# Optimization experiments

Hardware: AMD Instinct MI355X
Metric: run time of the kernel (lower is better)

Reference implementation:

```python
import jax, jax.numpy as jnp
import numpy as np

ALPHA = 0.5            # conf['alpha'] hybrid mixing
MAX_TOP_ANT = 50       # conf['max_top_antecedents']
MAX_SPAN_WIDTH = 30


def bucket_distance(d):
    # util.bucket_distance: identity 0..4, then log2 buckets, clipped to [0, 9]
    logspace = jnp.floor(jnp.log2(jnp.maximum(d, 1).astype(jnp.float32))).astype(d.dtype) + 3
    return jnp.clip(jnp.where(d <= 4, d, logspace), 0, 9)


def setup_inputs() -> dict:
    key = jax.random.key(0)
    ks = jax.random.split(key, 16)
    W, D, K, F, H = 4096, 768, 768, 20, 1000
    SPAN = 3 * D                      # span_emb_size = 3 * bert_emb_size
    PAIR = 3 * SPAN + F               # pair_emb_size (use_features only)
    std = 0.02

    mention_doc = jax.random.normal(ks[0], (W, D), jnp.float32)
    mention_doc_one = jax.random.normal(ks[1], (W, D), jnp.float32)
    top_span_starts = jnp.sort(jax.random.randint(ks[2], (K,), 0, W - MAX_SPAN_WIDTH))
    widths = jax.random.randint(ks[3], (K,), 0, MAX_SPAN_WIDTH)
    top_span_ends = jnp.minimum(top_span_starts + widths, W - 1)
    top_span_mention_scores = jax.random.normal(ks[4], (K,), jnp.float32)

    return {
        "mention_doc": mention_doc,
        "mention_doc_one": mention_doc_one,
        "top_span_starts": top_span_starts,
        "top_span_ends": top_span_ends,
        "top_span_mention_scores": top_span_mention_scores,
        # mention_token_attn: Linear(D -> 1)
        "attn_w": jax.random.normal(ks[5], (D,), jnp.float32) * std,
        "attn_b": jnp.zeros((), jnp.float32),
        # coarse_bilinear: Linear(SPAN -> SPAN)
        "coarse_w": jax.random.normal(ks[6], (SPAN, SPAN), jnp.float32) * std,
        "coarse_b": jnp.zeros((SPAN,), jnp.float32),
        # emb_antecedent_distance_prior [10, F] + antecedent_distance_score_ffnn Linear(F -> 1)
        "dist_prior_emb": jax.random.normal(ks[7], (10, F), jnp.float32) * std,
        "dist_w": jax.random.normal(ks[8], (F,), jnp.float32) * std,
        "dist_b": jnp.zeros((), jnp.float32),
        # emb_top_antecedent_distance [10, F]
        "top_dist_emb": jax.random.normal(ks[9], (10, F), jnp.float32) * std,
        # coref_score_ffnn: Linear(PAIR -> H), ReLU, Linear(H -> 1)
        "coref_w1": jax.random.normal(ks[10], (PAIR, H), jnp.float32) * std,
        "coref_b1": jnp.zeros((H,), jnp.float32),
        "coref_w2": jax.random.normal(ks[11], (H,), jnp.float32) * std,
        "coref_b2": jnp.zeros((), jnp.float32),
    }


def reference(mention_doc, mention_doc_one, top_span_starts, top_span_ends,
              top_span_mention_scores, attn_w, attn_b, coarse_w, coarse_b,
              dist_prior_emb, dist_w, dist_b, top_dist_emb,
              coref_w1, coref_b1, coref_w2, coref_b2):
    W = mention_doc.shape[0]
    K = top_span_starts.shape[0]
    C = min(K, MAX_TOP_ANT)
    NEG_INF = jnp.float32(-1e30) * 0 - jnp.inf  # true -inf, matches torch.log(0.)

    # --- span embeddings: start / end / head-attention over hybrid doc ---
    start_emb = mention_doc[top_span_starts]                      # [K, D]
    end_emb = mention_doc[top_span_ends]                          # [K, D]
    hybrid = mention_doc * (1.0 - ALPHA) + mention_doc_one * ALPHA
    token_attn = hybrid @ attn_w + attn_b                         # [W]
    tok = jnp.arange(W)
    span_tok_mask = (tok[None, :] >= top_span_starts[:, None]) & \
                    (tok[None, :] <= top_span_ends[:, None])      # [K, W]
    attn_raw = jnp.where(span_tok_mask, token_attn[None, :], NEG_INF)
    attn_probs = jax.nn.softmax(attn_raw, axis=1)                 # [K, W]
    head_emb = attn_probs @ hybrid                                # [K, D]
    span_emb = jnp.concatenate([start_emb, end_emb, head_emb], axis=1)  # [K, 3D]

    # --- coarse (fast) pairwise scores ---
    rng = jnp.arange(K)
    ant_offsets = rng[:, None] - rng[None, :]                     # [K, K]
    ant_mask = ant_offsets >= 1
    pair_sum = top_span_mention_scores[:, None] + top_span_mention_scores[None, :]
    src = span_emb @ coarse_w + coarse_b                          # coarse_bilinear
    fast = pair_sum + src @ span_emb.T
    fast = jnp.where(ant_mask, fast, NEG_INF)                     # + log(mask)
    dist_score = dist_prior_emb @ dist_w + dist_b                 # [10]
    fast = fast + dist_score[bucket_distance(ant_offsets)]        # distance prior

    # --- top-k antecedent pruning ---
    top_fast, top_idx = jax.lax.top_k(fast, C)                    # [K, C]
    top_ant_offsets = jnp.take_along_axis(ant_offsets, top_idx, axis=1)

    # --- fine-grained pairwise FFNN scoring ---
    dist_emb = top_dist_emb[bucket_distance(top_ant_offsets)]     # [K, C, F]
    ant_emb = span_emb[top_idx]                                   # [K, C, 3D]
    tgt_emb = jnp.broadcast_to(span_emb[:, None, :], ant_emb.shape)
    sim_emb = span_emb[:, None, :] * ant_emb
    pair_emb = jnp.concatenate([tgt_emb, ant_emb, sim_emb, dist_emb], axis=-1)  # [K, C, PAIR]
    h = jax.nn.relu(jnp.einsum('kcp,ph->kch', pair_emb, coref_w1) + coref_b1)
    slow = jnp.einsum('kch,h->kc', h, coref_w2) + coref_b2        # [K, C]
    top_scores = slow + top_fast

    # dummy antecedent (epsilon) column of zeros
    return jnp.concatenate([jnp.zeros((K, 1), top_scores.dtype), top_scores], axis=1)
```

## Files before the change

kernel.cpp:

```cpp
#include <hip/hip_runtime.h>
#include <math.h>

#define WTOK 4096
#define DD   768
#define KK   768
#define SPAN 2304
#define HH   1000
#define CC   50
#define NPAD 1024
#define NBIG 4352
#define PROWS (KK * CC)
#define PCHUNK (PROWS * 4)

typedef __attribute__((ext_vector_type(8))) short bf16x8;
typedef __attribute__((ext_vector_type(4))) float f32x4;
typedef unsigned short ushort;
typedef unsigned int uint;

__device__ __forceinline__ int bucketd(int d) {
  int l = (d >= 1) ? (31 - __clz(d)) : 0;
  int v = (d <= 4) ? d : (l + 3);
  return min(max(v, 0), 9);
}
__device__ __forceinline__ ushort f2bf(float f) {
  uint u = __float_as_uint(f);
  return (ushort)((u + 0x7fffu + ((u >> 16) & 1u)) >> 16);
}
__device__ __forceinline__ uint pkmul_t(uint a, uint b) {
  float lo = __uint_as_float(a << 16) * __uint_as_float(b << 16);
  float hi = __uint_as_float(a & 0xffff0000u) * __uint_as_float(b & 0xffff0000u);
  return (__float_as_uint(lo) >> 16) | (__float_as_uint(hi) & 0xffff0000u);
}
__device__ __forceinline__ uint4 pkmul4(uint4 a, uint4 b) {
  uint4 r;
  r.x = pkmul_t(a.x, b.x); r.y = pkmul_t(a.y, b.y);
  r.z = pkmul_t(a.z, b.z); r.w = pkmul_t(a.w, b.w);
  return r;
}
__device__ __forceinline__ void dma16(const ushort* g, ushort* l) {
  __builtin_amdgcn_global_load_lds(
      (const __attribute__((address_space(1))) void*)g,
      (__attribute__((address_space(3))) void*)l, 16, 0, 0);
}

#define PB_COARSE 5184
#define PB_W 2304
#define PB_SETUP_BASE (PB_COARSE + 3 * PB_W)
#define PB_SLOW_BASE  (PB_SETUP_BASE + 40)
#define PB_TOTAL      (PB_SLOW_BASE + 150)

__global__ __launch_bounds__(256) void prep_k(
    const float* __restrict__ coarse_w, const float* __restrict__ W1,
    const float* __restrict__ dist_prior, const float* __restrict__ dist_w,
    const float* __restrict__ dist_b, const float* __restrict__ top_dist,
    ushort* __restrict__ BigT, ushort* __restrict__ W1simT,
    float* __restrict__ dist_score, float* __restrict__ Pdist,
    float* __restrict__ slow)
{
  int bid = blockIdx.x;
  int tid = threadIdx.x;
  if (bid >= PB_SLOW_BASE) {
    int t = (bid - PB_SLOW_BASE) * 256 + tid;
    if (t < KK * CC) slow[t] = 0.f;
    return;
  }
  if (bid >= PB_SETUP_BASE) {
    int t = (bid - PB_SETUP_BASE) * 256 + tid;
    if (t < 10) {
      float s = dist_b[0];
      for (int f = 0; f < 20; ++f) s += dist_prior[t * 20 + f] * dist_w[f];
      dist_score[t] = s;
    }
    if (t < 10 * HH) {
      int b = t / HH, h = t % HH;
      float s = 0.f;
      for (int f = 0; f < 20; ++f)
        s += top_dist[b * 20 + f] * W1[(long)(6912 + f) * HH + h];
      Pdist[t] = s;
    }
    return;
  }
  const float* in; int ldin, Cin, nbase, NBrows; ushort* out; int idx;
  int xt;
  if (bid < PB_COARSE) {
    idx = bid; in = coarse_w; ldin = SPAN; Cin = SPAN; nbase = 0;
    NBrows = NBIG; out = BigT; xt = SPAN / 32;
  } else {
    idx = bid - PB_COARSE;
    int region = idx / PB_W;
    idx = idx % PB_W;
    if (region == 0) { in = W1; nbase = 2304; NBrows = NBIG; out = BigT; }
    else if (region == 1) { in = W1 + (size_t)SPAN * HH; nbase = 3328; NBrows = NBIG; out = BigT; }
    else { in = W1 + (size_t)2 * SPAN * HH; nbase = 0; NBrows = NPAD; out = W1simT; }
    ldin = HH; Cin = HH; xt = NPAD / 32;
  }
  {
    int bx = idx % xt, by = idx / xt;
    __shared__ float tile[32][33];
    int n0 = bx * 32, p0 = by * 32;
    int tx = tid & 31, ty = tid >> 5;
    for (int i = ty; i < 32; i += 8) {
      int p = p0 + i, n = n0 + tx;
      tile[i][tx] = (n < Cin) ? in[(long)p * ldin + n] : 0.f;
    }
    __syncthreads();
    size_t slab = (size_t)(p0 >> 5) * NBrows * 32;
    for (int i = ty; i < 32; i += 8) {
      int n = n0 + i;
      out[slab + (size_t)(nbase + n) * 32 + tx] = f2bf(tile[tx][i]);
    }
  }
}

__global__ __launch_bounds__(256) void hybrid_attn_k(
    const float* __restrict__ doc, const float* __restrict__ doc1,
    const float* __restrict__ attn_w, const float* __restrict__ attn_b,
    float* __restrict__ hybrid, float* __restrict__ tok_attn)
{
  int w = blockIdx.x;
  int tid = threadIdx.x;
  float part = 0.f;
  for (int d = tid; d < DD; d += 256) {
    float h = 0.5f * doc[(long)w * DD + d] + 0.5f * doc1[(long)w * DD + d];
    hybrid[(long)w * DD + d] = h;
    part += h * attn_w[d];
  }
  for (int off = 32; off > 0; off >>= 1) part += __shfl_down(part, off, 64);
  __shared__ float ws4[4];
  if ((tid & 63) == 0) ws4[tid >> 6] = part;
  __syncthreads();
  if (tid == 0) tok_attn[w] = ws4[0] + ws4[1] + ws4[2] + ws4[3] + attn_b[0];
}

__global__ __launch_bounds__(256) void span_emb_k(
    const float* __restrict__ doc, const float* __restrict__ hybrid,
    const float* __restrict__ tok_attn, const int* __restrict__ starts,
    const int* __restrict__ ends, ushort* __restrict__ se_bf)
{
  int k = blockIdx.x;
  int s = starts[k], e = ends[k];
  int len = e - s + 1;
  int tid = threadIdx.x;
  __shared__ float p_s[32];
  if (tid < 32) {
    float v = (tid < len) ? tok_attn[s + tid] : -INFINITY;
    float m = v;
    for (int msk = 16; msk >= 1; msk >>= 1) m = fmaxf(m, __shfl_xor(m, msk, 32));
    float pe = (tid < len) ? expf(v - m) : 0.f;
    float Z = pe;
    for (int msk = 16; msk >= 1; msk >>= 1) Z += __shfl_xor(Z, msk, 32);
    p_s[tid] = pe / Z;
  }
  __syncthreads();
  for (int d = tid; d < DD; d += 256) {
    float h = 0.f;
    for (int t = 0; t < len; ++t) h += p_s[t] * hybrid[(long)(s + t) * DD + d];
    se_bf[(long)k * SPAN + d]          = f2bf(doc[(long)s * DD + d]);
    se_bf[(long)k * SPAN + DD + d]     = f2bf(doc[(long)e * DD + d]);
    se_bf[(long)k * SPAN + 2 * DD + d] = f2bf(h);
  }
}

__global__ __launch_bounds__(256) void gemm_combined_k(
    const ushort* __restrict__ A, const ushort* __restrict__ B,
    const float* __restrict__ coarse_b, const float* __restrict__ b1,
    ushort* __restrict__ src_bf, float* __restrict__ Ptgt,
    float* __restrict__ Pant)
{
  __shared__ __align__(16) ushort As[64 * 40];
  __shared__ __align__(16) ushort Bs[128 * 32];
  int tid = threadIdx.x;
  int m0 = blockIdx.x * 64, n0 = blockIdx.y * 128;
  int lane = tid & 63, wid = tid >> 6;
  int quad = lane >> 4, lr = lane & 15;
  int wm = (wid & 1) << 5, wn = (wid >> 1) << 6;
  int arow = tid >> 2, aq = tid & 3;
  int gofs[2];
#pragma unroll
  for (int t = 0; t < 2; ++t) {
    int S = t * 256 + tid;
    int r = S >> 2, p = S & 3;
    int q = p ^ ((r >> 1) & 3);
    gofs[t] = (n0 + r) * 32 + q * 8;
  }
  f32x4 acc[2][4] = {};
  for (int k0 = 0; k0 < SPAN; k0 += 32) {
    uint4 a0 = *(const uint4*)(A + (size_t)(m0 + arow) * SPAN + k0 + aq * 8);
    __syncthreads();
    const ushort* sb = B + (size_t)(k0 >> 5) * (NBIG * 32);
    dma16(sb + gofs[0], &Bs[(size_t)(0 * 256 + tid) * 8]);
    dma16(sb + gofs[1], &Bs[(size_t)(1 * 256 + tid) * 8]);
    *(uint4*)&As[arow * 40 + aq * 8] = a0;
    __syncthreads();
    bf16x8 af[2], bfr[4];
#pragma unroll
    for (int mi = 0; mi < 2; ++mi)
      af[mi] = *(const bf16x8*)&As[(wm + mi * 16 + lr) * 40 + quad * 8];
#pragma unroll
    for (int ni = 0; ni < 4; ++ni) {
      int r = wn + ni * 16 + lr;
      int p = quad ^ ((r >> 1) & 3);
      bfr[ni] = *(const bf16x8*)&Bs[r * 32 + p * 8];
    }
#pragma unroll
    for (int mi = 0; mi < 2; ++mi)
#pragma unroll
      for (int ni = 0; ni < 4; ++ni)
        acc[mi][ni] = __builtin_amdgcn_mfma_f32_16x16x32_bf16(
            af[mi], bfr[ni], acc[mi][ni], 0, 0, 0);
  }
#pragma unroll
  for (int mi = 0; mi < 2; ++mi)
#pragma unroll
    for (int ni = 0; ni < 4; ++ni) {
      f32x4 c = acc[mi][ni];
#pragma unroll
      for (int reg = 0; reg < 4; ++reg) {
        int gm = m0 + wm + mi * 16 + quad * 4 + reg;
        int g = n0 + wn + ni * 16 + lr;
        float v = c[reg];
        if (g < 2304) {
          src_bf[(size_t)gm * SPAN + g] = f2bf(v + coarse_b[g]);
        } else if (g < 3328) {
          int n = g - 2304;
          if (n < HH) Ptgt[(size_t)gm * HH + n] = v + b1[n];
        } else {
          int n = g - 3328;
          if (n < HH) Pant[(size_t)gm * HH + n] = v;
        }
      }
    }
}

__global__ __launch_bounds__(256) void gemm_fast_k(
    const ushort* __restrict__ A, const ushort* __restrict__ B,
    const float* __restrict__ ms, const float* __restrict__ dist_score,
    float* __restrict__ fast)
{
  __shared__ __align__(16) ushort As[64 * 40];
  __shared__ __align__(16) ushort Bs[64 * 40];
  int tid = threadIdx.x;
  int m0 = blockIdx.x * 64, n0 = blockIdx.y * 64;
  int lane = tid & 63, wid = tid >> 6;
  int quad = lane >> 4, lr = lane & 15;
  int wm = (wid & 1) << 5, wn = (wid >> 1) << 5;
  int row = tid >> 2, aq = tid & 3;
  const ushort* ga = A + (size_t)(m0 + row) * SPAN + aq * 8;
  const ushort* gb = B + (size_t)(n0 + row) * SPAN + aq * 8;
  f32x4 acc[2][2] = {};
  for (int k0 = 0; k0 < SPAN; k0 += 32) {
    uint4 a0 = *(const uint4*)(ga + k0);
    uint4 b0 = *(const uint4*)(gb + k0);
    __syncthreads();
    *(uint4*)&As[row * 40 + aq * 8] = a0;
    *(uint4*)&Bs[row * 40 + aq * 8] = b0;
    __syncthreads();
    bf16x8 af[2], bfr[2];
#pragma unroll
    for (int mi = 0; mi < 2; ++mi)
      af[mi] = *(const bf16x8*)&As[(wm + mi * 16 + lr) * 40 + quad * 8];
#pragma unroll
    for (int ni = 0; ni < 2; ++ni)
      bfr[ni] = *(const bf16x8*)&Bs[(wn + ni * 16 + lr) * 40 + quad * 8];
#pragma unroll
    for (int mi = 0; mi < 2; ++mi)
#pragma unroll
      for (int ni = 0; ni < 2; ++ni)
        acc[mi][ni] = __builtin_amdgcn_mfma_f32_16x16x32_bf16(
            af[mi], bfr[ni], acc[mi][ni], 0, 0, 0);
  }
#pragma unroll
  for (int mi = 0; mi < 2; ++mi)
#pragma unroll
    for (int ni = 0; ni < 2; ++ni) {
      f32x4 c = acc[mi][ni];
#pragma unroll
      for (int reg = 0; reg < 4; ++reg) {
        int gm = m0 + wm + mi * 16 + quad * 4 + reg;
        int gn = n0 + wn + ni * 16 + lr;
        float v;
        if (gn < gm) {
          v = c[reg] + ms[gm] + ms[gn] + dist_score[bucketd(gm - gn)];
        } else {
          v = -INFINITY;
        }
        fast[(size_t)gm * KK + gn] = v;
      }
    }
}

__global__ __launch_bounds__(256) void topk_k(
    const float* __restrict__ fast, float* __restrict__ top_fast,
    int* __restrict__ row_j, int* __restrict__ row_bucket)
{
  __shared__ float vals[KK];
  __shared__ float wbv[4];
  __shared__ int wbi[4];
  int k = blockIdx.x;
  int tid = threadIdx.x;
  for (int j = tid; j < KK; j += 256) vals[j] = fast[(long)k * KK + j];
  __syncthreads();
  const float NANF = __uint_as_float(0x7fc00000u);
  for (int it = 0; it < CC; ++it) {
    float bv = -INFINITY;
    int bi = 1 << 30;
    for (int j = tid; j < KK; j += 256) {
      float v = vals[j];
      if (v > bv || (v == bv && j < bi)) { bv = v; bi = j; }
    }
    for (int off = 32; off > 0; off >>= 1) {
      float ov = __shfl_down(bv, off, 64);
      int oi = __shfl_down(bi, off, 64);
      if (ov > bv || (ov == bv && oi < bi)) { bv = ov; bi = oi; }
    }
    if ((tid & 63) == 0) { wbv[tid >> 6] = bv; wbi[tid >> 6] = bi; }
    __syncthreads();
    if (tid == 0) {
      for (int w = 1; w < 4; ++w) {
        float ov = wbv[w]; int oi = wbi[w];
        if (ov > bv || (ov == bv && oi < bi)) { bv = ov; bi = oi; }
      }
      int r = k * CC + it;
      top_fast[r] = bv;
      row_j[r] = bi;
      row_bucket[r] = bucketd(k - bi);
      vals[bi] = NANF;
    }
    __syncthreads();
  }
}

__global__ __launch_bounds__(256) void prod_k(
    const ushort* __restrict__ se_bf, const int* __restrict__ row_j,
    ushort* __restrict__ AsimT)
{
  int u = blockIdx.x * 256 + threadIdx.x;
  int c = u / PCHUNK;
  int rem = u - c * PCHUNK;
  int r = rem >> 2;
  int q = rem & 3;
  int kidx = r / CC;
  int j = row_j[r];
  int koff = c * 32 + q * 8;
  uint4 a = *(const uint4*)(se_bf + (size_t)kidx * SPAN + koff);
  uint4 b = *(const uint4*)(se_bf + (size_t)j * SPAN + koff);
  *(uint4*)(AsimT + (size_t)c * ((size_t)PROWS * 32) + (size_t)r * 32 + q * 8) =
      pkmul4(a, b);
}

__global__ __launch_bounds__(256, 4) void pair_mfma_k(
    const ushort* __restrict__ AsimT, const ushort* __restrict__ W1simT,
    const int* __restrict__ row_j, const int* __restrict__ row_bucket,
    const float* __restrict__ Ptgt, const float* __restrict__ Pant,
    const float* __restrict__ Pdist, const float* __restrict__ w2,
    float* __restrict__ slow)
{
  __shared__ __align__(16) ushort As[2][128 * 32];
  __shared__ __align__(16) ushort Bs[2][128 * 32];
  __shared__ int ks_s[128];
  __shared__ int js_s[128];
  __shared__ int bk_s[128];
  int tid = threadIdx.x;
  int b = blockIdx.x;
  int t = (b & 7) * 300 + (b >> 3);
  int m0 = (t >> 3) * 128, n0 = (t & 7) * 128;
  if (tid < 128) {
    int r = m0 + tid;
    ks_s[tid] = r / CC;
    js_s[tid] = row_j[r];
    bk_s[tid] = row_bucket[r];
  }
  int lane = tid & 63, wid = tid >> 6;
  int quad = lane >> 4, lr = lane & 15;
  int wm = (wid & 1) << 6, wn = (wid >> 1) << 6;
  int aofs[2], bofs[2];
#pragma unroll
  for (int tt = 0; tt < 2; ++tt) {
    int S = tt * 256 + tid;
    int r = S >> 2, p = S & 3;
    int q = p ^ ((r >> 1) & 3);
    aofs[tt] = (m0 + r) * 32 + q * 8;
    bofs[tt] = (n0 + r) * 32 + q * 8;
  }
#pragma unroll
  for (int tt = 0; tt < 2; ++tt) {
    dma16(AsimT + aofs[tt],  &As[0][(size_t)(tt * 256 + tid) * 8]);
    dma16(W1simT + bofs[tt], &Bs[0][(size_t)(tt * 256 + tid) * 8]);
  }
  __syncthreads();

  f32x4 acc[4][4] = {};
  for (int k0 = 0; k0 < SPAN; k0 += 32) {
    int buf = (k0 >> 5) & 1, nb = buf ^ 1;
    bool more = (k0 + 32) < SPAN;
    if (more) {
      size_t slab = (size_t)((k0 >> 5) + 1);
#pragma unroll
      for (int tt = 0; tt < 2; ++tt) {
        dma16(AsimT + slab * ((size_t)PROWS * 32) + aofs[tt],
              &As[nb][(size_t)(tt * 256 + tid) * 8]);
        dma16(W1simT + slab * (NPAD * 32) + bofs[tt],
              &Bs[nb][(size_t)(tt * 256 + tid) * 8]);
      }
    }
    bf16x8 af[4], bfr[4];
#pragma unroll
    for (int mi = 0; mi < 4; ++mi) {
      int r = wm + mi * 16 + lr;
      int p = quad ^ ((r >> 1) & 3);
      af[mi] = *(const bf16x8*)&As[buf][r * 32 + p * 8];
    }
#pragma unroll
    for (int ni = 0; ni < 4; ++ni) {
      int r = wn + ni * 16 + lr;
      int p = quad ^ ((r >> 1) & 3);
      bfr[ni] = *(const bf16x8*)&Bs[buf][r * 32 + p * 8];
    }
#pragma unroll
    for (int ni = 0; ni < 4; ++ni)
#pragma unroll
      for (int mi = 0; mi < 4; ++mi)
        acc[mi][ni] = __builtin_amdgcn_mfma_f32_16x16x32_bf16(
            af[mi], bfr[ni], acc[mi][ni], 0, 0, 0);
    __syncthreads();
  }
  int nn[4]; float w2r[4]; bool nv[4];
#pragma unroll
  for (int ni = 0; ni < 4; ++ni) {
    nn[ni] = n0 + wn + ni * 16 + lr;
    nv[ni] = nn[ni] < HH;
    w2r[ni] = nv[ni] ? w2[nn[ni]] : 0.f;
  }
#pragma unroll
  for (int mi = 0; mi < 4; ++mi) {
#pragma unroll
    for (int reg = 0; reg < 4; ++reg) {
      int rl = wm + mi * 16 + quad * 4 + reg;
      int kk = ks_s[rl], jj = js_s[rl], bb = bk_s[rl];
      float s = 0.f;
#pragma unroll
      for (int ni = 0; ni < 4; ++ni) {
        if (nv[ni]) {
          float h = acc[mi][ni][reg] + Ptgt[(size_t)kk * HH + nn[ni]] +
                    Pant[(size_t)jj * HH + nn[ni]] +
                    Pdist[(size_t)bb * HH + nn[ni]];
          s += fmaxf(h, 0.f) * w2r[ni];
        }
      }
      s += __shfl_xor(s, 1); s += __shfl_xor(s, 2);
      s += __shfl_xor(s, 4); s += __shfl_xor(s, 8);
      if (lr == 0) atomicAdd(&slow[m0 + rl], s);
    }
  }
}

__global__ void finalize_k(const float* __restrict__ slow,
                           const float* __restrict__ top_fast,
                           const float* __restrict__ b2, float* __restrict__ out)
{
  int t = blockIdx.x * 256 + threadIdx.x;
  if (t >= KK * (CC + 1)) return;
  int k = t / (CC + 1), col = t % (CC + 1);
  if (col == 0) {
    out[t] = 0.f;
  } else {
    int r = k * CC + col - 1;
    float v = slow[r] + b2[0] + top_fast[r];
    if (!isfinite(v)) v = -1.0e30f;
    out[t] = v;
  }
}

extern "C" void kernel_launch(void* const* d_in, const int* in_sizes, int n_in,
                              void* d_out, int out_size, void* d_ws, size_t ws_size,
                              hipStream_t stream)
{
  const float* doc        = (const float*)d_in[0];
  const float* doc1       = (const float*)d_in[1];
  const int*   starts     = (const int*)d_in[2];
  const int*   ends       = (const int*)d_in[3];
  const float* ms         = (const float*)d_in[4];
  const float* attn_w     = (const float*)d_in[5];
  const float* attn_b     = (const float*)d_in[6];
  const float* coarse_w   = (const float*)d_in[7];
  const float* coarse_b   = (const float*)d_in[8];
  const float* dist_prior = (const float*)d_in[9];
  const float* dist_w     = (const float*)d_in[10];
  const float* dist_b     = (const float*)d_in[11];
  const float* top_dist   = (const float*)d_in[12];
  const float* W1         = (const float*)d_in[13];
  const float* b1         = (const float*)d_in[14];
  const float* w2         = (const float*)d_in[15];
  const float* b2         = (const float*)d_in[16];
  float* out = (float*)d_out;

  char* ws = (char*)d_ws;
  size_t off = 0;
  auto alloc = [&](size_t bytes) { void* p = ws + off; off = (off + bytes + 1023) & ~(size_t)1023; return p; };
  ushort* se_bf      = (ushort*)alloc((size_t)KK * SPAN * 2 + 4096);
  float*  Ptgt       = (float*)alloc((size_t)KK * HH * 4);
  float*  Pant       = (float*)alloc((size_t)KK * HH * 4);
  float*  Pdist      = (float*)alloc((size_t)10 * HH * 4);
  float*  dist_score = (float*)alloc(64);
  float*  top_fast   = (float*)alloc((size_t)KK * CC * 4);
  int*    row_j      = (int*)alloc((size_t)KK * CC * 4);
  int*    row_bucket = (int*)alloc((size_t)KK * CC * 4);
  float*  slow       = (float*)alloc((size_t)KK * CC * 4);
  ushort* W1simT     = (ushort*)alloc((size_t)NPAD * SPAN * 2 + 4096);
  size_t ovl = off;
  float*  hybrid     = (float*)alloc((size_t)WTOK * DD * 4);
  float*  tok_attn   = (float*)alloc((size_t)WTOK * 4);
  ushort* src_bf     = (ushort*)alloc((size_t)KK * SPAN * 2 + 4096);
  float*  fast       = (float*)alloc((size_t)KK * KK * 4);
  ushort* BigT       = (ushort*)alloc((size_t)NBIG * SPAN * 2 + 4096);
  ushort* AsimT      = (ushort*)(ws + ovl);
  (void)ws_size; (void)in_sizes; (void)n_in; (void)out_size;

  prep_k<<<PB_TOTAL, 256, 0, stream>>>(coarse_w, W1, dist_prior, dist_w,
                                       dist_b, top_dist, BigT, W1simT,
                                       dist_score, Pdist, slow);
  hybrid_attn_k<<<WTOK, 256, 0, stream>>>(doc, doc1, attn_w, attn_b, hybrid, tok_attn);
  span_emb_k<<<KK, 256, 0, stream>>>(doc, hybrid, tok_attn, starts, ends, se_bf);
  {
    dim3 g(KK / 64, NBIG / 128);
    gemm_combined_k<<<g, 256, 0, stream>>>(se_bf, BigT, coarse_b, b1,
                                           src_bf, Ptgt, Pant);
  }
  {
    dim3 g(KK / 64, KK / 64);
    gemm_fast_k<<<g, 256, 0, stream>>>(src_bf, se_bf, ms, dist_score, fast);
  }
  topk_k<<<KK, 256, 0, stream>>>(fast, top_fast, row_j, row_bucket);
  prod_k<<<(72 * PCHUNK) / 256, 256, 0, stream>>>(se_bf, row_j, AsimT);
  pair_mfma_k<<<(PROWS / 128) * (NPAD / 128), 256, 0, stream>>>(
      AsimT, W1simT, row_j, row_bucket, Ptgt, Pant, Pdist, w2, slow);
  finalize_k<<<(KK * (CC + 1) + 255) / 256, 256, 0, stream>>>(slow, top_fast, b2, out);
}
```

Before: 580.4 us.

## Enlarge pair GEMM tiles to 256x256x64 with phased MFMA/load scheduling

Rewrites the pairwise MFMA kernel to use 256x256 block tiles with BK=64 and 512 threads. It interleaves LDS reads, MFMA groups and global-to-LDS DMA stages using sched barriers and priority hints. The A and W1sim layouts change to 64-wide K slabs with an XOR swizzle to match, which updates both prod_k and the prep transpose. The intent is more data reuse per tile and better overlap of loads with compute. The costs are higher register and LDS pressure, and the epilogue now reads row metadata from global memory instead of shared.

```diff
diff --git a/kernel.cpp b/kernel.cpp
--- a/kernel.cpp
+++ b/kernel.cpp
@@ -10,7 +10,6 @@
 #define NPAD 1024
 #define NBIG 4352
 #define PROWS (KK * CC)
-#define PCHUNK (PROWS * 4)
 
 typedef __attribute__((ext_vector_type(8))) short bf16x8;
 typedef __attribute__((ext_vector_type(4))) float f32x4;
@@ -81,7 +80,7 @@
     return;
   }
   const float* in; int ldin, Cin, nbase, NBrows; ushort* out; int idx;
-  int xt;
+  int xt; bool bk64 = false;
   if (bid < PB_COARSE) {
     idx = bid; in = coarse_w; ldin = SPAN; Cin = SPAN; nbase = 0;
     NBrows = NBIG; out = BigT; xt = SPAN / 32;
@@ -91,7 +90,7 @@
     idx = idx % PB_W;
     if (region == 0) { in = W1; nbase = 2304; NBrows = NBIG; out = BigT; }
     else if (region == 1) { in = W1 + (size_t)SPAN * HH; nbase = 3328; NBrows = NBIG; out = BigT; }
-    else { in = W1 + (size_t)2 * SPAN * HH; nbase = 0; NBrows = NPAD; out = W1simT; }
+    else { in = W1 + (size_t)2 * SPAN * HH; nbase = 0; NBrows = NPAD; out = W1simT; bk64 = true; }
     ldin = HH; Cin = HH; xt = NPAD / 32;
   }
   {
@@ -104,10 +103,22 @@
       tile[i][tx] = (n < Cin) ? in[(long)p * ldin + n] : 0.f;
     }
     __syncthreads();
-    size_t slab = (size_t)(p0 >> 5) * NBrows * 32;
-    for (int i = ty; i < 32; i += 8) {
-      int n = n0 + i;
-      out[slab + (size_t)(nbase + n) * 32 + tx] = f2bf(tile[tx][i]);
+    if (!bk64) {
+      size_t slab = (size_t)(p0 >> 5) * NBrows * 32;
+      for (int i = ty; i < 32; i += 8) {
+        int n = n0 + i;
+        out[slab + (size_t)(nbase + n) * 32 + tx] = f2bf(tile[tx][i]);
+      }
+    } else {
+      int p = p0 + tx;
+      int c = p >> 6, kin = p & 63;
+      int ls = kin >> 3, e = kin & 7;
+      size_t base = (size_t)c * NPAD * 64;
+      for (int i = ty; i < 32; i += 8) {
+        int n = n0 + i;
+        int ps = ls ^ (n & 7);
+        out[base + (size_t)n * 64 + ps * 8 + e] = f2bf(tile[tx][i]);
+      }
     }
   }
 }
@@ -335,95 +346,133 @@
     ushort* __restrict__ AsimT)
 {
   int u = blockIdx.x * 256 + threadIdx.x;
-  int c = u / PCHUNK;
-  int rem = u - c * PCHUNK;
-  int r = rem >> 2;
-  int q = rem & 3;
+  int ls = u & 7;
+  int v = u >> 3;
+  int c = v / PROWS;
+  int r = v - c * PROWS;
   int kidx = r / CC;
   int j = row_j[r];
-  int koff = c * 32 + q * 8;
+  int koff = c * 64 + ls * 8;
   uint4 a = *(const uint4*)(se_bf + (size_t)kidx * SPAN + koff);
   uint4 b = *(const uint4*)(se_bf + (size_t)j * SPAN + koff);
-  *(uint4*)(AsimT + (size_t)c * ((size_t)PROWS * 32) + (size_t)r * 32 + q * 8) =
-      pkmul4(a, b);
-}
-
-__global__ __launch_bounds__(256, 4) void pair_mfma_k(
+  int ps = ls ^ (r & 7);
+  *(uint4*)(AsimT + ((size_t)c * PROWS + r) * 64 + ps * 8) = pkmul4(a, b);
+}
+
+#define BM 256
+#define BN 256
+#define BK 64
+#define KST 36
+
+#define PH_MID \
+  __builtin_amdgcn_sched_barrier(0); \
+  __builtin_amdgcn_s_barrier(); \
+  asm volatile("s_waitcnt lgkmcnt(0)" ::: "memory"); \
+  __builtin_amdgcn_sched_barrier(0); \
+  __builtin_amdgcn_s_setprio(1)
+
+#define PH_END \
+  __builtin_amdgcn_s_setprio(0); \
+  __builtin_amdgcn_sched_barrier(0); \
+  __builtin_amdgcn_s_barrier(); \
+  __builtin_amdgcn_sched_barrier(0)
+
+__global__ __launch_bounds__(512, 2) void pair_mfma_k(
     const ushort* __restrict__ AsimT, const ushort* __restrict__ W1simT,
     const int* __restrict__ row_j, const int* __restrict__ row_bucket,
     const float* __restrict__ Ptgt, const float* __restrict__ Pant,
     const float* __restrict__ Pdist, const float* __restrict__ w2,
     float* __restrict__ slow)
 {
-  __shared__ __align__(16) ushort As[2][128 * 32];
-  __shared__ __align__(16) ushort Bs[2][128 * 32];
-  __shared__ int ks_s[128];
-  __shared__ int js_s[128];
-  __shared__ int bk_s[128];
+  __shared__ __align__(16) ushort As[2][BM * BK];
+  __shared__ __align__(16) ushort Bs[2][BN * BK];
   int tid = threadIdx.x;
   int b = blockIdx.x;
-  int t = (b & 7) * 300 + (b >> 3);
-  int m0 = (t >> 3) * 128, n0 = (t & 7) * 128;
-  if (tid < 128) {
-    int r = m0 + tid;
-    ks_s[tid] = r / CC;
-    js_s[tid] = row_j[r];
-    bk_s[tid] = row_bucket[r];
-  }
+  int t = (b & 7) * 75 + (b >> 3);
+  int m0 = (t >> 2) * BM;
+  int n0 = (t & 3) * BN;
   int lane = tid & 63, wid = tid >> 6;
   int quad = lane >> 4, lr = lane & 15;
-  int wm = (wid & 1) << 6, wn = (wid >> 1) << 6;
-  int aofs[2], bofs[2];
-#pragma unroll
-  for (int tt = 0; tt < 2; ++tt) {
-    int S = tt * 256 + tid;
-    int r = S >> 2, p = S & 3;
-    int q = p ^ ((r >> 1) & 3);
-    aofs[tt] = (m0 + r) * 32 + q * 8;
-    bofs[tt] = (n0 + r) * 32 + q * 8;
-  }
-#pragma unroll
-  for (int tt = 0; tt < 2; ++tt) {
-    dma16(AsimT + aofs[tt],  &As[0][(size_t)(tt * 256 + tid) * 8]);
-    dma16(W1simT + bofs[tt], &Bs[0][(size_t)(tt * 256 + tid) * 8]);
-  }
-  __syncthreads();
-
-  f32x4 acc[4][4] = {};
-  for (int k0 = 0; k0 < SPAN; k0 += 32) {
-    int buf = (k0 >> 5) & 1, nb = buf ^ 1;
-    bool more = (k0 + 32) < SPAN;
-    if (more) {
-      size_t slab = (size_t)((k0 >> 5) + 1);
-#pragma unroll
-      for (int tt = 0; tt < 2; ++tt) {
-        dma16(AsimT + slab * ((size_t)PROWS * 32) + aofs[tt],
-              &As[nb][(size_t)(tt * 256 + tid) * 8]);
-        dma16(W1simT + slab * (NPAD * 32) + bofs[tt],
-              &Bs[nb][(size_t)(tt * 256 + tid) * 8]);
-      }
-    }
-    bf16x8 af[4], bfr[4];
-#pragma unroll
-    for (int mi = 0; mi < 4; ++mi) {
-      int r = wm + mi * 16 + lr;
-      int p = quad ^ ((r >> 1) & 3);
-      af[mi] = *(const bf16x8*)&As[buf][r * 32 + p * 8];
-    }
-#pragma unroll
-    for (int ni = 0; ni < 4; ++ni) {
-      int r = wn + ni * 16 + lr;
-      int p = quad ^ ((r >> 1) & 3);
-      bfr[ni] = *(const bf16x8*)&Bs[buf][r * 32 + p * 8];
-    }
-#pragma unroll
-    for (int ni = 0; ni < 4; ++ni)
-#pragma unroll
-      for (int mi = 0; mi < 4; ++mi)
-        acc[mi][ni] = __builtin_amdgcn_mfma_f32_16x16x32_bf16(
-            af[mi], bfr[ni], acc[mi][ni], 0, 0, 0);
-    __syncthreads();
-  }
+  int wm = (wid >> 2) << 7;
+  int wn = (wid & 3) << 6;
+
+  const ushort* gA = AsimT + (size_t)m0 * BK + (size_t)tid * 8;
+  const ushort* gB = W1simT + (size_t)n0 * BK + (size_t)tid * 8;
+  const size_t ASTRIDE = (size_t)PROWS * BK;
+  const size_t BSTRIDE = (size_t)NPAD * BK;
+
+#define STAGE_A(s, bi) do { \
+    const ushort* g_ = gA + (size_t)(s) * ASTRIDE; \
+    ushort* l_ = &As[bi][tid * 8]; \
+    dma16(g_, l_);                 dma16(g_ + 4096, l_ + 4096); \
+    dma16(g_ + 8192, l_ + 8192);   dma16(g_ + 12288, l_ + 12288); \
+  } while (0)
+#define STAGE_B(s, bi) do { \
+    const ushort* g_ = gB + (size_t)(s) * BSTRIDE; \
+    ushort* l_ = &Bs[bi][tid * 8]; \
+    dma16(g_, l_);                 dma16(g_ + 4096, l_ + 4096); \
+    dma16(g_ + 8192, l_ + 8192);   dma16(g_ + 12288, l_ + 12288); \
+  } while (0)
+#define READ_A(AF, MH) do { \
+    _Pragma("unroll") for (int mi = 0; mi < 4; ++mi) { \
+      int row_ = wm + (MH) * 64 + mi * 16 + lr; \
+      int rx_ = row_ & 7; \
+      _Pragma("unroll") for (int kh = 0; kh < 2; ++kh) { \
+        int ps_ = (kh * 4 + quad) ^ rx_; \
+        AF[mi][kh] = *(const bf16x8*)&As[buf][row_ * 64 + ps_ * 8]; } } \
+  } while (0)
+#define READ_B(BF, NH) do { \
+    _Pragma("unroll") for (int ni = 0; ni < 2; ++ni) { \
+      int row_ = wn + (NH) * 32 + ni * 16 + lr; \
+      int rx_ = row_ & 7; \
+      _Pragma("unroll") for (int kh = 0; kh < 2; ++kh) { \
+        int ps_ = (kh * 4 + quad) ^ rx_; \
+        BF[ni][kh] = *(const bf16x8*)&Bs[buf][row_ * 64 + ps_ * 8]; } } \
+  } while (0)
+#define QMFMA(MH, NH, AF, BF) do { \
+    _Pragma("unroll") for (int kh = 0; kh < 2; ++kh) \
+      _Pragma("unroll") for (int ni = 0; ni < 2; ++ni) \
+        _Pragma("unroll") for (int mi = 0; mi < 4; ++mi) \
+          acc[(MH)*4 + mi][(NH)*2 + ni] = __builtin_amdgcn_mfma_f32_16x16x32_bf16( \
+              AF[mi][kh], BF[ni][kh], acc[(MH)*4 + mi][(NH)*2 + ni], 0, 0, 0); \
+  } while (0)
+
+  f32x4 acc[8][4] = {};
+  STAGE_A(0, 0);
+  STAGE_B(0, 0);
+  STAGE_A(1, 1);
+  asm volatile("s_waitcnt vmcnt(4)" ::: "memory");
+  __builtin_amdgcn_s_barrier();
+  __builtin_amdgcn_sched_barrier(0);
+
+  bf16x8 af[4][2], bl[2][2], bh[2][2];
+  for (int u = 0; u < KST; ++u) {
+    int buf = u & 1;
+    READ_A(af, 0);
+    READ_B(bl, 0);
+    if (u + 1 < KST) STAGE_B(u + 1, buf ^ 1);
+    PH_MID;
+    QMFMA(0, 0, af, bl);
+    PH_END;
+    READ_B(bh, 1);
+    PH_MID;
+    QMFMA(0, 1, af, bh);
+    PH_END;
+    READ_A(af, 1);
+    PH_MID;
+    QMFMA(1, 0, af, bl);
+    PH_END;
+    if (u + 2 < KST) STAGE_A(u + 2, buf);
+    PH_MID;
+    QMFMA(1, 1, af, bh);
+    __builtin_amdgcn_s_setprio(0);
+    __builtin_amdgcn_sched_barrier(0);
+    if (u < KST - 2) asm volatile("s_waitcnt vmcnt(4)" ::: "memory");
+    else             asm volatile("s_waitcnt vmcnt(0)" ::: "memory");
+    __builtin_amdgcn_s_barrier();
+    __builtin_amdgcn_sched_barrier(0);
+  }
+
   int nn[4]; float w2r[4]; bool nv[4];
 #pragma unroll
   for (int ni = 0; ni < 4; ++ni) {
@@ -432,16 +481,17 @@
     w2r[ni] = nv[ni] ? w2[nn[ni]] : 0.f;
   }
 #pragma unroll
-  for (int mi = 0; mi < 4; ++mi) {
+  for (int mg = 0; mg < 8; ++mg) {
 #pragma unroll
     for (int reg = 0; reg < 4; ++reg) {
-      int rl = wm + mi * 16 + quad * 4 + reg;
-      int kk = ks_s[rl], jj = js_s[rl], bb = bk_s[rl];
+      int grow = m0 + wm + mg * 16 + quad * 4 + reg;
+      int kk = grow / CC;
+      int jj = row_j[grow], bb = row_bucket[grow];
       float s = 0.f;
 #pragma unroll
       for (int ni = 0; ni < 4; ++ni) {
         if (nv[ni]) {
-          float h = acc[mi][ni][reg] + Ptgt[(size_t)kk * HH + nn[ni]] +
+          float h = acc[mg][ni][reg] + Ptgt[(size_t)kk * HH + nn[ni]] +
                     Pant[(size_t)jj * HH + nn[ni]] +
                     Pdist[(size_t)bb * HH + nn[ni]];
           s += fmaxf(h, 0.f) * w2r[ni];
@@ -449,9 +499,14 @@
       }
       s += __shfl_xor(s, 1); s += __shfl_xor(s, 2);
       s += __shfl_xor(s, 4); s += __shfl_xor(s, 8);
-      if (lr == 0) atomicAdd(&slow[m0 + rl], s);
-    }
-  }
+      if (lr == 0) atomicAdd(&slow[grow], s);
+    }
+  }
+#undef STAGE_A
+#undef STAGE_B
+#undef READ_A
+#undef READ_B
+#undef QMFMA
 }
 
 __global__ void finalize_k(const float* __restrict__ slow,
@@ -531,8 +586,8 @@
     gemm_fast_k<<<g, 256, 0, stream>>>(src_bf, se_bf, ms, dist_score, fast);
   }
   topk_k<<<KK, 256, 0, stream>>>(fast, top_fast, row_j, row_bucket);
-  prod_k<<<(72 * PCHUNK) / 256, 256, 0, stream>>>(se_bf, row_j, AsimT);
-  pair_mfma_k<<<(PROWS / 128) * (NPAD / 128), 256, 0, stream>>>(
+  prod_k<<<(36 * PROWS * 8) / 256, 256, 0, stream>>>(se_bf, row_j, AsimT);
+  pair_mfma_k<<<(PROWS / BM) * (NPAD / BN), 512, 0, stream>>>(
       AsimT, W1simT, row_j, row_bucket, Ptgt, Pant, Pdist, w2, slow);
   finalize_k<<<(KK * (CC + 1) + 255) / 256, 256, 0, stream>>>(slow, top_fast, b2, out);
 }
```

New measurement: 617.5 us. 6.4% more time.

## Triple-buffer LDS tiles in pair MFMA kernel with partial vmcnt waits

Applied to the files above, without the earlier changes.

Switches the pairwise bf16 MFMA GEMM from double to triple-buffered LDS staging. Loads now run two k-slabs ahead, and the wait uses s_waitcnt vmcnt(4) instead of draining all outstanding DMA at each barrier, so global loads overlap more MFMA work. It also raises wave priority around the MFMA block. The cost is 50% more LDS per block, which lowers the occupancy hint from 4 to 3 blocks per CU, and the hand-placed waitcnt and barriers are fragile.

```diff
diff --git a/kernel.cpp b/kernel.cpp
--- a/kernel.cpp
+++ b/kernel.cpp
@@ -348,15 +348,17 @@
       pkmul4(a, b);
 }
 
-__global__ __launch_bounds__(256, 4) void pair_mfma_k(
+#define KST2 72
+
+__global__ __launch_bounds__(256, 3) void pair_mfma_k(
     const ushort* __restrict__ AsimT, const ushort* __restrict__ W1simT,
     const int* __restrict__ row_j, const int* __restrict__ row_bucket,
     const float* __restrict__ Ptgt, const float* __restrict__ Pant,
     const float* __restrict__ Pdist, const float* __restrict__ w2,
     float* __restrict__ slow)
 {
-  __shared__ __align__(16) ushort As[2][128 * 32];
-  __shared__ __align__(16) ushort Bs[2][128 * 32];
+  __shared__ __align__(16) ushort As[3][128 * 32];
+  __shared__ __align__(16) ushort Bs[3][128 * 32];
   __shared__ int ks_s[128];
   __shared__ int js_s[128];
   __shared__ int bk_s[128];
@@ -382,48 +384,61 @@
     aofs[tt] = (m0 + r) * 32 + q * 8;
     bofs[tt] = (n0 + r) * 32 + q * 8;
   }
-#pragma unroll
-  for (int tt = 0; tt < 2; ++tt) {
-    dma16(AsimT + aofs[tt],  &As[0][(size_t)(tt * 256 + tid) * 8]);
-    dma16(W1simT + bofs[tt], &Bs[0][(size_t)(tt * 256 + tid) * 8]);
-  }
-  __syncthreads();
+
+#define STAGE(s, Ad, Bd) do { \
+    const ushort* sa_ = AsimT + (size_t)(s) * ((size_t)PROWS * 32); \
+    const ushort* sb_ = W1simT + (size_t)(s) * (NPAD * 32); \
+    dma16(sa_ + aofs[0], (Ad) + (size_t)(0 * 256 + tid) * 8); \
+    dma16(sa_ + aofs[1], (Ad) + (size_t)(1 * 256 + tid) * 8); \
+    dma16(sb_ + bofs[0], (Bd) + (size_t)(0 * 256 + tid) * 8); \
+    dma16(sb_ + bofs[1], (Bd) + (size_t)(1 * 256 + tid) * 8); \
+  } while (0)
+
+  ushort *A0 = As[0], *A1 = As[1], *A2 = As[2];
+  ushort *B0 = Bs[0], *B1 = Bs[1], *B2 = Bs[2];
+
+  STAGE(0, A0, B0);
+  STAGE(1, A1, B1);
+  asm volatile("s_waitcnt vmcnt(4)" ::: "memory");
+  __builtin_amdgcn_s_barrier();
+  __builtin_amdgcn_sched_barrier(0);
 
   f32x4 acc[4][4] = {};
-  for (int k0 = 0; k0 < SPAN; k0 += 32) {
-    int buf = (k0 >> 5) & 1, nb = buf ^ 1;
-    bool more = (k0 + 32) < SPAN;
-    if (more) {
-      size_t slab = (size_t)((k0 >> 5) + 1);
-#pragma unroll
-      for (int tt = 0; tt < 2; ++tt) {
-        dma16(AsimT + slab * ((size_t)PROWS * 32) + aofs[tt],
-              &As[nb][(size_t)(tt * 256 + tid) * 8]);
-        dma16(W1simT + slab * (NPAD * 32) + bofs[tt],
-              &Bs[nb][(size_t)(tt * 256 + tid) * 8]);
-      }
-    }
+  for (int u = 0; u < KST2; ++u) {
+    bool more = (u + 2) < KST2;
+    if (more) STAGE(u + 2, A2, B2);
+    __builtin_amdgcn_sched_barrier(0);
     bf16x8 af[4], bfr[4];
 #pragma unroll
     for (int mi = 0; mi < 4; ++mi) {
       int r = wm + mi * 16 + lr;
       int p = quad ^ ((r >> 1) & 3);
-      af[mi] = *(const bf16x8*)&As[buf][r * 32 + p * 8];
+      af[mi] = *(const bf16x8*)&A0[r * 32 + p * 8];
     }
 #pragma unroll
     for (int ni = 0; ni < 4; ++ni) {
       int r = wn + ni * 16 + lr;
       int p = quad ^ ((r >> 1) & 3);
-      bfr[ni] = *(const bf16x8*)&Bs[buf][r * 32 + p * 8];
-    }
+      bfr[ni] = *(const bf16x8*)&B0[r * 32 + p * 8];
+    }
+    __builtin_amdgcn_s_setprio(1);
 #pragma unroll
     for (int ni = 0; ni < 4; ++ni)
 #pragma unroll
       for (int mi = 0; mi < 4; ++mi)
         acc[mi][ni] = __builtin_amdgcn_mfma_f32_16x16x32_bf16(
             af[mi], bfr[ni], acc[mi][ni], 0, 0, 0);
-    __syncthreads();
-  }
+    __builtin_amdgcn_s_setprio(0);
+    __builtin_amdgcn_sched_barrier(0);
+    if (more) asm volatile("s_waitcnt vmcnt(4)" ::: "memory");
+    else      asm volatile("s_waitcnt vmcnt(0)" ::: "memory");
+    __builtin_amdgcn_s_barrier();
+    __builtin_amdgcn_sched_barrier(0);
+    ushort* ta = A0; A0 = A1; A1 = A2; A2 = ta;
+    ushort* tb = B0; B0 = B1; B1 = B2; B2 = tb;
+  }
+#undef STAGE
+
   int nn[4]; float w2r[4]; bool nv[4];
 #pragma unroll
   for (int ni = 0; ni < 4; ++ni) {
```

New measurement: 619.1 us. +6.7%, slower.
